# Kernel optimization log

Measured on AMD Instinct MI355X. Metric: run time of the kernel, lower is better.

Reference implementation:

```python
import jax, jax.numpy as jnp
import numpy as np

NA, NP_, E = 40000, 60000, 80000
D, H = 512, 8
DK = D // H
SQRT_DK = float(DK) ** 0.5


def setup_inputs() -> dict:
    key = jax.random.key(0)
    ks = list(jax.random.split(key, 20))
    it = iter(ks)

    def nrm(shape, scale=1.0):
        return jax.random.normal(next(it), shape, dtype=jnp.float32) * scale

    xav = (6.0 / (DK + DK)) ** 0.5  # xavier_uniform bound for (dk, dk)
    w_scale = D ** -0.5
    inp = {
        "h_author": nrm((NA, D)),
        "h_paper": nrm((NP_, D)),
        "writes_src": jax.random.randint(next(it), (E,), 0, NA, dtype=jnp.int32),
        "writes_dst": jax.random.randint(next(it), (E,), 0, NP_, dtype=jnp.int32),
        "cites_src": jax.random.randint(next(it), (E,), 0, NP_, dtype=jnp.int32),
        "cites_dst": jax.random.randint(next(it), (E,), 0, NP_, dtype=jnp.int32),
        "wb_src": jax.random.randint(next(it), (E,), 0, NP_, dtype=jnp.int32),
        "wb_dst": jax.random.randint(next(it), (E,), 0, NA, dtype=jnp.int32),
        # per-node-type linear weights (2 types: 0=author, 1=paper)
        "Wk": nrm((2, D, D), w_scale), "bk": jnp.zeros((2, D), jnp.float32),
        "Wq": nrm((2, D, D), w_scale), "bq": jnp.zeros((2, D), jnp.float32),
        "Wv": nrm((2, D, D), w_scale), "bv": jnp.zeros((2, D), jnp.float32),
        "Wa": nrm((2, D, D), w_scale), "ba": jnp.zeros((2, D), jnp.float32),
        # per-relation params (3 relations: 0=writes, 1=cites, 2=written_by)
        "rel_att": jax.random.uniform(next(it), (3, H, DK, DK), jnp.float32, -xav, xav),
        "rel_msg": jax.random.uniform(next(it), (3, H, DK, DK), jnp.float32, -xav, xav),
        "rel_pri": jnp.ones((3, H), jnp.float32),
        "skip": jnp.ones((2,), jnp.float32),
    }
    return inp


def _edge_attn_agg(k, q, v, src, dst, pri, n_dst):
    # k, v: (N_src, H, DK) relation-transformed; q: (N_dst, H, DK)
    s = jnp.einsum('ehd,ehd->eh', q[dst], k[src]) * pri / SQRT_DK  # (E, H)
    m = jax.ops.segment_max(s, dst, num_segments=n_dst)            # edge softmax by dst
    ex = jnp.exp(s - m[dst])
    den = jax.ops.segment_sum(ex, dst, num_segments=n_dst)
    a = ex / den[dst]
    return jax.ops.segment_sum(v[src] * a[:, :, None], dst, num_segments=n_dst)


def reference(h_author, h_paper, writes_src, writes_dst, cites_src, cites_dst,
              wb_src, wb_dst, Wk, bk, Wq, bq, Wv, bv, Wa, ba,
              rel_att, rel_msg, rel_pri, skip):
    def proj(h, W, b, t):
        return (h @ W[t] + b[t]).reshape(-1, H, DK)

    k_a, v_a, q_a = proj(h_author, Wk, bk, 0), proj(h_author, Wv, bv, 0), proj(h_author, Wq, bq, 0)
    k_p, v_p, q_p = proj(h_paper, Wk, bk, 1), proj(h_paper, Wv, bv, 1), proj(h_paper, Wq, bq, 1)

    def rel(k, v, r):
        return (jnp.einsum('nhd,hde->nhe', k, rel_att[r]),
                jnp.einsum('nhd,hde->nhe', v, rel_msg[r]))

    k0, v0 = rel(k_a, v_a, 0)  # writes: author -> paper
    agg_w = _edge_attn_agg(k0, q_p, v0, writes_src, writes_dst, rel_pri[0], NP_)
    k1, v1 = rel(k_p, v_p, 1)  # cites: paper -> paper
    agg_c = _edge_attn_agg(k1, q_p, v1, cites_src, cites_dst, rel_pri[1], NP_)
    k2, v2 = rel(k_p, v_p, 2)  # written_by: paper -> author
    agg_b = _edge_attn_agg(k2, q_a, v2, wb_src, wb_dst, rel_pri[2], NA)

    t_paper = ((agg_w + agg_c) * 0.5).reshape(NP_, D)  # cross_reducer='mean'
    t_author = agg_b.reshape(NA, D)

    alpha = jax.nn.sigmoid(skip)
    out_a = (t_author @ Wa[0] + ba[0]) * alpha[0] + h_author * (1.0 - alpha[0])
    out_p = (t_paper @ Wa[1] + ba[1]) * alpha[1] + h_paper * (1.0 - alpha[1])
    return out_a, out_p
```

## Files before the change

kernel.cpp:

```cpp
#include <hip/hip_runtime.h>
#include <math.h>

#define D_ 512
#define H_ 8

typedef short bf16x8 __attribute__((ext_vector_type(8)));
typedef float f32x4 __attribute__((ext_vector_type(4)));

struct Outs { void* p[5]; };

__device__ __forceinline__ unsigned short f2bf(float x) {
  unsigned int u = __float_as_uint(x);
  unsigned int r = (u + 0x7fff + ((u >> 16) & 1)) >> 16;
  return (unsigned short)r;
}
__device__ __forceinline__ float bf2f(unsigned short b) {
  return __uint_as_float(((unsigned int)b) << 16);
}

__global__ void fill_kernel(float* __restrict__ p, float v, long n) {
  long i = (long)blockIdx.x * blockDim.x + threadIdx.x;
  long st = (long)gridDim.x * blockDim.x;
  for (; i < n; i += st) p[i] = v;
}

__global__ void convert_bf16_kernel(const float* __restrict__ in,
                                    unsigned short* __restrict__ out, long n8) {
  long i = (long)blockIdx.x * blockDim.x + threadIdx.x;
  long st = (long)gridDim.x * blockDim.x;
  for (; i < n8; i += st) {
    float4 a = ((const float4*)in)[i * 2];
    float4 b = ((const float4*)in)[i * 2 + 1];
    bf16x8 o;
    o[0] = (short)f2bf(a.x); o[1] = (short)f2bf(a.y);
    o[2] = (short)f2bf(a.z); o[3] = (short)f2bf(a.w);
    o[4] = (short)f2bf(b.x); o[5] = (short)f2bf(b.y);
    o[6] = (short)f2bf(b.z); o[7] = (short)f2bf(b.w);
    ((bf16x8*)out)[i] = o;
  }
}

__global__ void transpose_bf16_kernel(const float* __restrict__ W,
                                      unsigned short* __restrict__ Wt) {
  int n = blockIdx.x;
  int k = threadIdx.x;
  Wt[(long)n * D_ + k] = f2bf(W[(long)k * D_ + n]);
}

__global__ void copy_bias_kernel(const float* __restrict__ in,
                                 float* __restrict__ out) {
  out[threadIdx.x] = in[threadIdx.x];
}

__global__ void fuse_weight_kernel(const float* __restrict__ Win,
                                   const float* __restrict__ bin,
                                   const float* __restrict__ rel,
                                   unsigned short* __restrict__ Wf,
                                   float* __restrict__ bf) {
  int row = blockIdx.x;
  int j = threadIdx.x;
  int h = j >> 6, e = j & 63;
  const float* src = (row < D_) ? (Win + (long)row * D_) : bin;
  const float* rl = rel + h * 64 * 64;
  float acc = 0.f;
#pragma unroll 16
  for (int d = 0; d < 64; ++d) acc = fmaf(src[h * 64 + d], rl[d * 64 + e], acc);
  if (row < D_) Wf[(long)j * D_ + row] = f2bf(acc);
  else bf[j] = acc;
}

__global__ void hist_kernel(const int* __restrict__ w_dst,
                            const int* __restrict__ c_dst,
                            const int* __restrict__ b_dst,
                            int* __restrict__ degree, int E, int NP) {
  int i = blockIdx.x * blockDim.x + threadIdx.x;
  if (i >= 3 * E) return;
  int r = i / E, e = i - r * E;
  int d, base;
  if (r == 0)      { d = w_dst[e]; base = 0; }
  else if (r == 1) { d = c_dst[e]; base = NP; }
  else             { d = b_dst[e]; base = 2 * NP; }
  atomicAdd(degree + base + d, 1);
}

__global__ void scan1_kernel(const int* __restrict__ in, int* __restrict__ out,
                             int* __restrict__ aux, int n) {
  __shared__ int tmp[256];
  int t = threadIdx.x;
  int i = blockIdx.x * 256 + t;
  int v = (i < n) ? in[i] : 0;
  tmp[t] = v;
  __syncthreads();
#pragma unroll
  for (int d = 1; d < 256; d <<= 1) {
    int add = (t >= d) ? tmp[t - d] : 0;
    __syncthreads();
    tmp[t] += add;
    __syncthreads();
  }
  if (i < n) out[i] = tmp[t] - v;
  if (t == 255) aux[blockIdx.x] = tmp[255];
}

__global__ void scan2_kernel(int* __restrict__ aux, int nb) {
  __shared__ int tmp[1024];
  int t = threadIdx.x;
  int v = (t < nb) ? aux[t] : 0;
  tmp[t] = v;
  __syncthreads();
#pragma unroll
  for (int d = 1; d < 1024; d <<= 1) {
    int add = (t >= d) ? tmp[t - d] : 0;
    __syncthreads();
    tmp[t] += add;
    __syncthreads();
  }
  if (t < nb) aux[t] = tmp[t] - v;
}

__global__ void scan3_kernel(int* __restrict__ starts, int* __restrict__ cursor,
                             const int* __restrict__ aux, int n) {
  int i = blockIdx.x * 256 + threadIdx.x;
  if (i >= n) return;
  int s = starts[i] + aux[blockIdx.x];
  starts[i] = s;
  cursor[i] = s;
}

__global__ void scatter_kernel(const int* __restrict__ w_src, const int* __restrict__ w_dst,
                               const int* __restrict__ c_src, const int* __restrict__ c_dst,
                               const int* __restrict__ b_src, const int* __restrict__ b_dst,
                               int* __restrict__ cursor, int* __restrict__ csr,
                               int E, int NP) {
  int i = blockIdx.x * blockDim.x + threadIdx.x;
  if (i >= 3 * E) return;
  int r = i / E, e = i - r * E;
  int s, d, base;
  if (r == 0)      { s = w_src[e]; d = w_dst[e]; base = 0; }
  else if (r == 1) { s = c_src[e]; d = c_dst[e]; base = NP; }
  else             { s = b_src[e]; d = b_dst[e]; base = 2 * NP; }
  int pos = atomicAdd(cursor + base + d, 1);
  csr[pos] = s;
}

template <int TWO_LISTS>
__global__ __launch_bounds__(256) void attn_kernel(
    const unsigned short* __restrict__ q,
    const unsigned short* __restrict__ k0, const unsigned short* __restrict__ v0,
    const unsigned short* __restrict__ k1, const unsigned short* __restrict__ v1,
    const int* __restrict__ csr, const int* __restrict__ starts,
    const int* __restrict__ degree, int base0, int base1,
    const float* __restrict__ pri, int poff0, int poff1,
    unsigned short* __restrict__ out, int n_nodes, float outscale) {
  int gw = (int)(((long)blockIdx.x * blockDim.x + threadIdx.x) >> 6);
  if (gw >= n_nodes) return;
  int lane = threadIdx.x & 63;
  int h = lane >> 3, off = (lane & 7) << 3;
  const long rowoff = (long)gw * D_ + h * 64 + off;
  bf16x8 qv = *(const bf16x8*)(q + rowoff);
  float qf[8];
#pragma unroll
  for (int r = 0; r < 8; ++r) qf[r] = bf2f((unsigned short)qv[r]);

  float res[8] = {};

  auto process = [&](const unsigned short* K, const unsigned short* V,
                     int base, float ps) {
    int st = starts[base + gw], dg = degree[base + gw];
    float m = -INFINITY, l = 0.f;
    float acc[8] = {};
    for (int i = 0; i < dg; ++i) {
      int s = csr[st + i];
      const long ro = (long)s * D_ + h * 64 + off;
      bf16x8 kv = *(const bf16x8*)(K + ro);
      bf16x8 vv = *(const bf16x8*)(V + ro);
      float dot = 0.f;
#pragma unroll
      for (int r = 0; r < 8; ++r)
        dot = fmaf(qf[r], bf2f((unsigned short)kv[r]), dot);
      dot += __shfl_xor(dot, 1);
      dot += __shfl_xor(dot, 2);
      dot += __shfl_xor(dot, 4);
      float sc = dot * ps;
      float mn = fmaxf(m, sc);
      float scale = __expf(m - mn);
      float p = __expf(sc - mn);
      l = l * scale + p;
#pragma unroll
      for (int r = 0; r < 8; ++r)
        acc[r] = acc[r] * scale + p * bf2f((unsigned short)vv[r]);
      m = mn;
    }
    if (l > 0.f) {
      float inv = 1.f / l;
#pragma unroll
      for (int r = 0; r < 8; ++r) res[r] += acc[r] * inv;
    }
  };

  process(k0, v0, base0, pri[poff0 + h] * 0.125f);
  if (TWO_LISTS) process(k1, v1, base1, pri[poff1 + h] * 0.125f);

  bf16x8 o;
#pragma unroll
  for (int r = 0; r < 8; ++r) o[r] = (short)f2bf(res[r] * outscale);
  *(bf16x8*)(out + rowoff) = o;
}

__device__ __forceinline__ void gload_lds16(const void* g, void* l) {
  __builtin_amdgcn_global_load_lds(
      (const __attribute__((address_space(1))) void*)g,
      (__attribute__((address_space(3))) void*)l, 16, 0, 0);
}

template <int OUT_BF16, int WITH_SKIP>
__global__ __launch_bounds__(512, 2) void gemm_mfma(
    const unsigned short* __restrict__ A,
    const unsigned short* __restrict__ Bt,
    const float* __restrict__ bias,
    Outs outs, int M, int GX, float a_scale,
    const float* __restrict__ Hres,
    const float* __restrict__ skip, int skip_idx) {
  __shared__ unsigned short Asm[2][256 * 64];
  __shared__ unsigned short Bsm[2][256 * 64];

  const int nwg = gridDim.x;
  const int orig = blockIdx.x;
  const int q8 = nwg >> 3, r8 = nwg & 7;
  const int xcd = orig & 7, pos = orig >> 3;
  const int wgid =
      (xcd < r8 ? xcd * (q8 + 1) : r8 * (q8 + 1) + (xcd - r8) * q8) + pos;
  const int bm = (wgid / GX) * 256;
  const int bn = (wgid % GX) * 256;

  const int tid = threadIdx.x;
  const int wave = tid >> 6, lane = tid & 63;
  const int wm = (wave >> 2) * 128;
  const int wn = (wave & 3) * 64;
  const int srow = tid >> 3;
  const int swz = ((tid & 7) ^ (srow & 7)) * 8;

  f32x4 acc[8][4] = {};

  const int rr = lane & 15;
  const int rx = (rr & 7) << 4;

  auto STAGE = [&](int buf, int kt) {
    const int k0 = kt * 64;
#pragma unroll
    for (int i = 0; i < 4; ++i) {
      int gr = bm + srow + i * 64;
      if (gr >= M) gr = M - 1;
      gload_lds16(A + (long)gr * D_ + k0 + swz, &Asm[buf][i * 4096 + wave * 512]);
    }
#pragma unroll
    for (int i = 0; i < 4; ++i) {
      int gr = bn + srow + i * 64;
      gload_lds16(Bt + (long)gr * D_ + k0 + swz, &Bsm[buf][i * 4096 + wave * 512]);
    }
  };

  STAGE(0, 0);
  STAGE(1, 1);

#pragma unroll
  for (int t = 0; t < 8; ++t) {
    const int p = t & 1;
    if (t == 7) asm volatile("s_waitcnt vmcnt(0)" ::: "memory");
    else        asm volatile("s_waitcnt vmcnt(8)" ::: "memory");
    __builtin_amdgcn_s_barrier();
    asm volatile("" ::: "memory");

#pragma unroll
    for (int kk = 0; kk < 2; ++kk) {
      const int cb = kk * 64 + (lane >> 4) * 16;
      const int cs = cb ^ rx;
      bf16x8 af[8], bfr[4];
#pragma unroll
      for (int mi = 0; mi < 8; ++mi)
        af[mi] = *(const bf16x8*)((const char*)&Asm[p][0] +
                                  (wm + mi * 16 + rr) * 128 + cs);
#pragma unroll
      for (int nj = 0; nj < 4; ++nj)
        bfr[nj] = *(const bf16x8*)((const char*)&Bsm[p][0] +
                                   (wn + nj * 16 + rr) * 128 + cs);
      __builtin_amdgcn_s_setprio(1);
#pragma unroll
      for (int mi = 0; mi < 8; ++mi)
#pragma unroll
        for (int nj = 0; nj < 4; ++nj)
          acc[mi][nj] = __builtin_amdgcn_mfma_f32_16x16x32_bf16(
              af[mi], bfr[nj], acc[mi][nj], 0, 0, 0);
      __builtin_amdgcn_s_setprio(0);
    }

    asm volatile("" ::: "memory");
    __builtin_amdgcn_s_barrier();
    asm volatile("" ::: "memory");
    if (t + 2 < 8) STAGE(p, t + 2);
  }

  float alpha = 1.f, beta = 0.f;
  if (WITH_SKIP) {
    float sv = skip[skip_idx];
    alpha = 1.f / (1.f + expf(-sv));
    beta = 1.f - alpha;
  }
  const int cr = (lane >> 4) * 4;
  const int cc = lane & 15;
  const int matu = (bn + wn) >> 9;
  const int wcb = (bn + wn) & 511;
  unsigned short* ob16 = (unsigned short*)outs.p[matu];
  float* ob32 = (float*)outs.p[0];
#pragma unroll
  for (int mi = 0; mi < 8; ++mi) {
    int rowb = bm + wm + mi * 16 + cr;
#pragma unroll
    for (int nj = 0; nj < 4; ++nj) {
      int col = bn + wn + nj * 16 + cc;
      float bb = bias[col];
#pragma unroll
      for (int r = 0; r < 4; ++r) {
        int row = rowb + r;
        if (row >= M) continue;
        float val = acc[mi][nj][r] * a_scale + bb;
        if (WITH_SKIP) val = val * alpha + Hres[(long)row * D_ + col] * beta;
        if (OUT_BF16)
          ob16[(long)row * D_ + wcb + nj * 16 + cc] = f2bf(val);
        else
          ob32[(long)row * D_ + col] = val;
      }
    }
  }
}

extern "C" void kernel_launch(void* const* d_in, const int* in_sizes, int n_in,
                              void* d_out, int out_size, void* d_ws, size_t ws_size,
                              hipStream_t stream) {
  const float* h_author = (const float*)d_in[0];
  const float* h_paper  = (const float*)d_in[1];
  const int* w_src = (const int*)d_in[2];
  const int* w_dst = (const int*)d_in[3];
  const int* c_src = (const int*)d_in[4];
  const int* c_dst = (const int*)d_in[5];
  const int* b_src = (const int*)d_in[6];
  const int* b_dst = (const int*)d_in[7];
  const float* Wk = (const float*)d_in[8];
  const float* bk = (const float*)d_in[9];
  const float* Wq = (const float*)d_in[10];
  const float* bq = (const float*)d_in[11];
  const float* Wv = (const float*)d_in[12];
  const float* bv = (const float*)d_in[13];
  const float* Wa = (const float*)d_in[14];
  const float* ba = (const float*)d_in[15];
  const float* rel_att = (const float*)d_in[16];
  const float* rel_msg = (const float*)d_in[17];
  const float* rel_pri = (const float*)d_in[18];
  const float* skip = (const float*)d_in[19];

  const int NA = in_sizes[0] / D_;
  const int NP = in_sizes[1] / D_;
  const int E  = in_sizes[2];
  const long nmax = (NA > NP) ? NA : NP;
  const int NT = 2 * NP + NA;

  char* w = (char*)d_ws;
  auto alloc = [&](long bytes) {
    char* p = w;
    w += (bytes + 255) & ~255L;
    return p;
  };
  unsigned short* hA16 = (unsigned short*)alloc((long)NA * D_ * 2);
  unsigned short* hP16 = (unsigned short*)alloc((long)NP * D_ * 2);
  unsigned short* Pq   = (unsigned short*)alloc((long)NP * D_ * 2);
  unsigned short* Pkc  = (unsigned short*)alloc((long)NP * D_ * 2);
  unsigned short* Pvc  = (unsigned short*)alloc((long)NP * D_ * 2);
  unsigned short* Pkb  = (unsigned short*)alloc((long)NP * D_ * 2);
  unsigned short* Pvb  = (unsigned short*)alloc((long)NP * D_ * 2);
  unsigned short* Aq   = (unsigned short*)alloc((long)NA * D_ * 2);
  unsigned short* Akw  = (unsigned short*)alloc((long)NA * D_ * 2);
  unsigned short* Avw  = (unsigned short*)alloc((long)NA * D_ * 2);
  unsigned short* t16  = (unsigned short*)alloc(nmax * D_ * 2);
  unsigned short* BtP  = (unsigned short*)alloc((long)2560 * D_ * 2);
  unsigned short* BtA  = (unsigned short*)alloc((long)1536 * D_ * 2);
  float* bfP           = (float*)alloc(2560 * 4);
  float* bfA           = (float*)alloc(1536 * 4);
  unsigned short* Wa0t = (unsigned short*)alloc((long)D_ * D_ * 2);
  unsigned short* Wa1t = (unsigned short*)alloc((long)D_ * D_ * 2);
  int* degree          = (int*)alloc((long)NT * 4);
  int* starts          = (int*)alloc((long)NT * 4);
  int* cursor          = (int*)alloc((long)NT * 4);
  int* csr             = (int*)alloc((long)3 * E * 4);
  int* aux             = (int*)alloc(((long)NT / 256 + 2) * 4);

  const long WD = (long)D_ * D_;
  const long RS = (long)H_ * 64 * 64;
  const long SEG = (long)D_ * D_;

  auto fill = [&](float* p, float v, long n) {
    long b = (n + 255) / 256;
    int blocks = (int)(b > 4096 ? 4096 : b);
    fill_kernel<<<blocks, 256, 0, stream>>>(p, v, n);
  };
  auto cvt = [&](const float* in, unsigned short* out, long n) {
    long n8 = n / 8;
    long b = (n8 + 255) / 256;
    int blocks = (int)(b > 2048 ? 2048 : b);
    convert_bf16_kernel<<<blocks, 256, 0, stream>>>(in, out, n8);
  };

  float* out_a = (float*)d_out;
  float* out_p = out_a + (long)NA * D_;

  cvt(h_author, hA16, (long)NA * D_);
  cvt(h_paper, hP16, (long)NP * D_);

  fill((float*)degree, 0.f, NT);
  {
    int th = 3 * E;
    hist_kernel<<<(th + 255) / 256, 256, 0, stream>>>(w_dst, c_dst, b_dst,
                                                      degree, E, NP);
    int nb = (NT + 255) / 256;
    scan1_kernel<<<nb, 256, 0, stream>>>(degree, starts, aux, NT);
    scan2_kernel<<<1, 1024, 0, stream>>>(aux, nb);
    scan3_kernel<<<nb, 256, 0, stream>>>(starts, cursor, aux, NT);
    scatter_kernel<<<(th + 255) / 256, 256, 0, stream>>>(
        w_src, w_dst, c_src, c_dst, b_src, b_dst, cursor, csr, E, NP);
  }

  transpose_bf16_kernel<<<D_, D_, 0, stream>>>(Wq + WD, BtP);
  copy_bias_kernel<<<1, D_, 0, stream>>>(bq + D_, bfP);
  fuse_weight_kernel<<<513, 512, 0, stream>>>(Wk + WD, bk + D_, rel_att + RS,
                                              BtP + SEG, bfP + 512);
  fuse_weight_kernel<<<513, 512, 0, stream>>>(Wv + WD, bv + D_, rel_msg + RS,
                                              BtP + 2 * SEG, bfP + 1024);
  fuse_weight_kernel<<<513, 512, 0, stream>>>(Wk + WD, bk + D_, rel_att + 2 * RS,
                                              BtP + 3 * SEG, bfP + 1536);
  fuse_weight_kernel<<<513, 512, 0, stream>>>(Wv + WD, bv + D_, rel_msg + 2 * RS,
                                              BtP + 4 * SEG, bfP + 2048);

  transpose_bf16_kernel<<<D_, D_, 0, stream>>>(Wq, BtA);
  copy_bias_kernel<<<1, D_, 0, stream>>>(bq, bfA);
  fuse_weight_kernel<<<513, 512, 0, stream>>>(Wk, bk, rel_att,
                                              BtA + SEG, bfA + 512);
  fuse_weight_kernel<<<513, 512, 0, stream>>>(Wv, bv, rel_msg,
                                              BtA + 2 * SEG, bfA + 1024);

  transpose_bf16_kernel<<<D_, D_, 0, stream>>>(Wa, Wa0t);
  transpose_bf16_kernel<<<D_, D_, 0, stream>>>(Wa + WD, Wa1t);

  {
    Outs o; o.p[0] = Pq; o.p[1] = Pkc; o.p[2] = Pvc; o.p[3] = Pkb; o.p[4] = Pvb;
    int gy = (NP + 255) / 256;
    gemm_mfma<1, 0><<<10 * gy, 512, 0, stream>>>(
        hP16, BtP, bfP, o, NP, 10, 1.f, nullptr, nullptr, 0);
  }
  {
    Outs o; o.p[0] = Aq; o.p[1] = Akw; o.p[2] = Avw; o.p[3] = Aq; o.p[4] = Aq;
    int gy = (NA + 255) / 256;
    gemm_mfma<1, 0><<<6 * gy, 512, 0, stream>>>(
        hA16, BtA, bfA, o, NA, 6, 1.f, nullptr, nullptr, 0);
  }

  {
    long th = (long)NP * 64;
    attn_kernel<1><<<(int)((th + 255) / 256), 256, 0, stream>>>(
        Pq, Akw, Avw, Pkc, Pvc, csr, starts, degree, 0, NP,
        rel_pri, 0, H_, t16, NP, 0.5f);
  }
  {
    Outs o; o.p[0] = out_p; o.p[1] = o.p[2] = o.p[3] = o.p[4] = out_p;
    int gy = (NP + 255) / 256;
    gemm_mfma<0, 1><<<2 * gy, 512, 0, stream>>>(
        t16, Wa1t, ba + D_, o, NP, 2, 1.f, h_paper, skip, 1);
  }

  {
    long th = (long)NA * 64;
    attn_kernel<0><<<(int)((th + 255) / 256), 256, 0, stream>>>(
        Aq, Pkb, Pvb, Pkb, Pvb, csr, starts, degree, 2 * NP, 2 * NP,
        rel_pri, 2 * H_, 2 * H_, t16, NA, 1.f);
  }
  {
    Outs o; o.p[0] = out_a; o.p[1] = o.p[2] = o.p[3] = o.p[4] = out_a;
    int gy = (NA + 255) / 256;
    gemm_mfma<0, 1><<<2 * gy, 512, 0, stream>>>(
        t16, Wa0t, ba, o, NA, 2, 1.f, h_author, skip, 0);
  }
}
```

Before: 985.5 us.

## Deepen MFMA GEMM LDS pipeline to 3-ahead half-K stages with one barrier

Splits each 64-wide K tile of the bf16 MFMA GEMM into two 32-wide halves held in four LDS slots. It prefetches three stages ahead and issues the next global-to-LDS load right after fragment reads, so only one barrier per step remains instead of two. The LDS layout changes to 64-byte rows with a new XOR swizzle. The aim is to hide global load latency better and cut synchronisation stalls. The costs are more loop iterations with smaller MFMA batches per barrier, plus possible bank-conflict changes from the new swizzle.

```diff
diff --git a/kernel.cpp b/kernel.cpp
--- a/kernel.cpp
+++ b/kernel.cpp
@@ -221,8 +221,8 @@
     Outs outs, int M, int GX, float a_scale,
     const float* __restrict__ Hres,
     const float* __restrict__ skip, int skip_idx) {
-  __shared__ unsigned short Asm[2][256 * 64];
-  __shared__ unsigned short Bsm[2][256 * 64];
+  __shared__ unsigned short AsmL[4 * 8192];
+  __shared__ unsigned short BsmL[4 * 8192];
 
   const int nwg = gridDim.x;
   const int orig = blockIdx.x;
@@ -237,67 +237,73 @@
   const int wave = tid >> 6, lane = tid & 63;
   const int wm = (wave >> 2) * 128;
   const int wn = (wave & 3) * 64;
-  const int srow = tid >> 3;
-  const int swz = ((tid & 7) ^ (srow & 7)) * 8;
+
+  const int srow = tid >> 2;
+  const int schk = tid & 3;
+  const int sf = ((tid >> 2) & 3) ^ ((tid >> 4) & 3);
+  const int scg = ((schk ^ sf) << 3);
+
+  const int rr = lane & 15;
+  const int qk = lane >> 4;
+  const int slotx = ((qk ^ (rr & 3) ^ ((rr >> 2) & 3)) << 4);
 
   f32x4 acc[8][4] = {};
 
-  const int rr = lane & 15;
-  const int rx = (rr & 7) << 4;
-
-  auto STAGE = [&](int buf, int kt) {
-    const int k0 = kt * 64;
-#pragma unroll
-    for (int i = 0; i < 4; ++i) {
-      int gr = bm + srow + i * 64;
+  auto STAGE_U = [&](int u) {
+    const int tile = u >> 1, kh = u & 1;
+    const int slot = ((tile & 1) * 2 + kh);
+    const int k0 = tile * 64 + kh * 32 + scg;
+#pragma unroll
+    for (int rd = 0; rd < 2; ++rd) {
+      int gr = bm + srow + rd * 128;
       if (gr >= M) gr = M - 1;
-      gload_lds16(A + (long)gr * D_ + k0 + swz, &Asm[buf][i * 4096 + wave * 512]);
+      gload_lds16(A + (long)gr * D_ + k0,
+                  AsmL + slot * 8192 + rd * 4096 + wave * 512);
     }
 #pragma unroll
-    for (int i = 0; i < 4; ++i) {
-      int gr = bn + srow + i * 64;
-      gload_lds16(Bt + (long)gr * D_ + k0 + swz, &Bsm[buf][i * 4096 + wave * 512]);
+    for (int rd = 0; rd < 2; ++rd) {
+      int gr = bn + srow + rd * 128;
+      gload_lds16(Bt + (long)gr * D_ + k0,
+                  BsmL + slot * 8192 + rd * 4096 + wave * 512);
     }
   };
 
-  STAGE(0, 0);
-  STAGE(1, 1);
-
-#pragma unroll
-  for (int t = 0; t < 8; ++t) {
-    const int p = t & 1;
-    if (t == 7) asm volatile("s_waitcnt vmcnt(0)" ::: "memory");
-    else        asm volatile("s_waitcnt vmcnt(8)" ::: "memory");
+  STAGE_U(0);
+  STAGE_U(1);
+  STAGE_U(2);
+
+#pragma unroll
+  for (int s = 0; s < 16; ++s) {
+    if (s <= 13)      asm volatile("s_waitcnt vmcnt(8)" ::: "memory");
+    else if (s == 14) asm volatile("s_waitcnt vmcnt(4)" ::: "memory");
+    else              asm volatile("s_waitcnt vmcnt(0)" ::: "memory");
     __builtin_amdgcn_s_barrier();
     asm volatile("" ::: "memory");
 
-#pragma unroll
-    for (int kk = 0; kk < 2; ++kk) {
-      const int cb = kk * 64 + (lane >> 4) * 16;
-      const int cs = cb ^ rx;
-      bf16x8 af[8], bfr[4];
-#pragma unroll
-      for (int mi = 0; mi < 8; ++mi)
-        af[mi] = *(const bf16x8*)((const char*)&Asm[p][0] +
-                                  (wm + mi * 16 + rr) * 128 + cs);
+    const int tile = s >> 1, kh = s & 1;
+    const int slot = ((tile & 1) * 2 + kh);
+    const char* ab = (const char*)AsmL + slot * 16384;
+    const char* bb = (const char*)BsmL + slot * 16384;
+
+    bf16x8 af[8], bfr[4];
+#pragma unroll
+    for (int mi = 0; mi < 8; ++mi)
+      af[mi] = *(const bf16x8*)(ab + (wm + mi * 16 + rr) * 64 + slotx);
+#pragma unroll
+    for (int nj = 0; nj < 4; ++nj)
+      bfr[nj] = *(const bf16x8*)(bb + (wn + nj * 16 + rr) * 64 + slotx);
+
+    if (s + 3 <= 15) STAGE_U(s + 3);
+
+    __builtin_amdgcn_s_setprio(1);
+#pragma unroll
+    for (int mi = 0; mi < 8; ++mi)
 #pragma unroll
       for (int nj = 0; nj < 4; ++nj)
-        bfr[nj] = *(const bf16x8*)((const char*)&Bsm[p][0] +
-                                   (wn + nj * 16 + rr) * 128 + cs);
-      __builtin_amdgcn_s_setprio(1);
-#pragma unroll
-      for (int mi = 0; mi < 8; ++mi)
-#pragma unroll
-        for (int nj = 0; nj < 4; ++nj)
-          acc[mi][nj] = __builtin_amdgcn_mfma_f32_16x16x32_bf16(
-              af[mi], bfr[nj], acc[mi][nj], 0, 0, 0);
-      __builtin_amdgcn_s_setprio(0);
-    }
-
+        acc[mi][nj] = __builtin_amdgcn_mfma_f32_16x16x32_bf16(
+            af[mi], bfr[nj], acc[mi][nj], 0, 0, 0);
+    __builtin_amdgcn_s_setprio(0);
     asm volatile("" ::: "memory");
-    __builtin_amdgcn_s_barrier();
-    asm volatile("" ::: "memory");
-    if (t + 2 < 8) STAGE(p, t + 2);
   }
 
   float alpha = 1.f, beta = 0.f;
@@ -318,12 +324,12 @@
 #pragma unroll
     for (int nj = 0; nj < 4; ++nj) {
       int col = bn + wn + nj * 16 + cc;
-      float bb = bias[col];
+      float bb2 = bias[col];
 #pragma unroll
       for (int r = 0; r < 4; ++r) {
         int row = rowb + r;
         if (row >= M) continue;
-        float val = acc[mi][nj][r] * a_scale + bb;
+        float val = acc[mi][nj][r] * a_scale + bb2;
         if (WITH_SKIP) val = val * alpha + Hres[(long)row * D_ + col] * beta;
         if (OUT_BF16)
           ob16[(long)row * D_ + wcb + nj * 16 + cc] = f2bf(val);
```

After: 1.002 ms. About the same (+1.6%).

## Merge prep, projection, attention and output launches into grouped kernels

Applied to the files above, without the earlier changes.

Folds the bf16 conversions, weight fusion, transposes, bias copies and degree zeroing into one multi-role prep kernel. The two projection GEMMs, the two attention passes and the two output GEMMs each become a single grouped launch. A padded shared t16 buffer lets author and paper rows coexist. This cuts launch count and tail under-utilisation, at the cost of more complex index dispatch and a larger workspace.

```diff
diff --git a/kernel.cpp b/kernel.cpp
--- a/kernel.cpp
+++ b/kernel.cpp
@@ -6,8 +6,6 @@
 
 typedef short bf16x8 __attribute__((ext_vector_type(8)));
 typedef float f32x4 __attribute__((ext_vector_type(4)));
-
-struct Outs { void* p[5]; };
 
 __device__ __forceinline__ unsigned short f2bf(float x) {
   unsigned int u = __float_as_uint(x);
@@ -18,55 +16,58 @@
   return __uint_as_float(((unsigned int)b) << 16);
 }
 
-__global__ void fill_kernel(float* __restrict__ p, float v, long n) {
-  long i = (long)blockIdx.x * blockDim.x + threadIdx.x;
-  long st = (long)gridDim.x * blockDim.x;
-  for (; i < n; i += st) p[i] = v;
-}
-
-__global__ void convert_bf16_kernel(const float* __restrict__ in,
-                                    unsigned short* __restrict__ out, long n8) {
-  long i = (long)blockIdx.x * blockDim.x + threadIdx.x;
-  long st = (long)gridDim.x * blockDim.x;
-  for (; i < n8; i += st) {
+struct PrepArgs {
+  const float *hA, *hP;
+  unsigned short *hA16, *hP16;
+  const float *fWin[6], *fbin[6], *frel[6];
+  unsigned short *fWf[6];
+  float *fbf[6];
+  const float *tW[4];
+  unsigned short *tWt[4];
+  const float *cin[2];
+  float *cout[2];
+  int *degree;
+  int NT;
+  int b1, b2, b3, b4, b5;
+};
+
+__global__ __launch_bounds__(512) void prep_kernel(PrepArgs p) {
+  const int b = blockIdx.x, t = threadIdx.x;
+  if (b < p.b2) {
+    const float* in; unsigned short* out; long i;
+    if (b < p.b1) { in = p.hA; out = p.hA16; i = (long)b * 512 + t; }
+    else          { in = p.hP; out = p.hP16; i = (long)(b - p.b1) * 512 + t; }
     float4 a = ((const float4*)in)[i * 2];
-    float4 b = ((const float4*)in)[i * 2 + 1];
+    float4 c = ((const float4*)in)[i * 2 + 1];
     bf16x8 o;
     o[0] = (short)f2bf(a.x); o[1] = (short)f2bf(a.y);
     o[2] = (short)f2bf(a.z); o[3] = (short)f2bf(a.w);
-    o[4] = (short)f2bf(b.x); o[5] = (short)f2bf(b.y);
-    o[6] = (short)f2bf(b.z); o[7] = (short)f2bf(b.w);
+    o[4] = (short)f2bf(c.x); o[5] = (short)f2bf(c.y);
+    o[6] = (short)f2bf(c.z); o[7] = (short)f2bf(c.w);
     ((bf16x8*)out)[i] = o;
-  }
-}
-
-__global__ void transpose_bf16_kernel(const float* __restrict__ W,
-                                      unsigned short* __restrict__ Wt) {
-  int n = blockIdx.x;
-  int k = threadIdx.x;
-  Wt[(long)n * D_ + k] = f2bf(W[(long)k * D_ + n]);
-}
-
-__global__ void copy_bias_kernel(const float* __restrict__ in,
-                                 float* __restrict__ out) {
-  out[threadIdx.x] = in[threadIdx.x];
-}
-
-__global__ void fuse_weight_kernel(const float* __restrict__ Win,
-                                   const float* __restrict__ bin,
-                                   const float* __restrict__ rel,
-                                   unsigned short* __restrict__ Wf,
-                                   float* __restrict__ bf) {
-  int row = blockIdx.x;
-  int j = threadIdx.x;
-  int h = j >> 6, e = j & 63;
-  const float* src = (row < D_) ? (Win + (long)row * D_) : bin;
-  const float* rl = rel + h * 64 * 64;
-  float acc = 0.f;
+  } else if (b < p.b3) {
+    int idx = b - p.b2;
+    int job = idx / 513, row = idx - job * 513;
+    int h = t >> 6, e = t & 63;
+    const float* src = (row < D_) ? (p.fWin[job] + (long)row * D_) : p.fbin[job];
+    const float* rl = p.frel[job] + h * 64 * 64;
+    float acc = 0.f;
 #pragma unroll 16
-  for (int d = 0; d < 64; ++d) acc = fmaf(src[h * 64 + d], rl[d * 64 + e], acc);
-  if (row < D_) Wf[(long)j * D_ + row] = f2bf(acc);
-  else bf[j] = acc;
+    for (int d = 0; d < 64; ++d)
+      acc = fmaf(src[h * 64 + d], rl[d * 64 + e], acc);
+    if (row < D_) p.fWf[job][(long)t * D_ + row] = f2bf(acc);
+    else p.fbf[job][t] = acc;
+  } else if (b < p.b4) {
+    int idx = b - p.b3;
+    int job = idx >> 9, n = idx & 511;
+    p.tWt[job][(long)n * D_ + t] = f2bf(p.tW[job][(long)t * D_ + n]);
+  } else if (b < p.b5) {
+    int job = b - p.b4;
+    p.cout[job][t] = p.cin[job][t];
+  } else {
+    int i = (b - p.b5) * 512 + t;
+    if (i < p.NT) p.degree[i] = 0;
+  }
 }
 
 __global__ void hist_kernel(const int* __restrict__ w_dst,
@@ -143,21 +144,42 @@
   csr[pos] = s;
 }
 
-template <int TWO_LISTS>
-__global__ __launch_bounds__(256) void attn_kernel(
-    const unsigned short* __restrict__ q,
-    const unsigned short* __restrict__ k0, const unsigned short* __restrict__ v0,
-    const unsigned short* __restrict__ k1, const unsigned short* __restrict__ v1,
+__global__ __launch_bounds__(256) void attn_all(
+    const unsigned short* __restrict__ Pq,
+    const unsigned short* __restrict__ Akw, const unsigned short* __restrict__ Avw,
+    const unsigned short* __restrict__ Pkc, const unsigned short* __restrict__ Pvc,
+    const unsigned short* __restrict__ Aq,
+    const unsigned short* __restrict__ Pkb, const unsigned short* __restrict__ Pvb,
     const int* __restrict__ csr, const int* __restrict__ starts,
-    const int* __restrict__ degree, int base0, int base1,
-    const float* __restrict__ pri, int poff0, int poff1,
-    unsigned short* __restrict__ out, int n_nodes, float outscale) {
-  int gw = (int)(((long)blockIdx.x * blockDim.x + threadIdx.x) >> 6);
-  if (gw >= n_nodes) return;
+    const int* __restrict__ degree, const float* __restrict__ pri,
+    unsigned short* __restrict__ t16, int NP, int NA, int NAp) {
+  long gid = (long)blockIdx.x * blockDim.x + threadIdx.x;
+  int gw = (int)(gid >> 6);
+  if (gw >= NP + NAp) return;
   int lane = threadIdx.x & 63;
   int h = lane >> 3, off = (lane & 7) << 3;
-  const long rowoff = (long)gw * D_ + h * 64 + off;
-  bf16x8 qv = *(const bf16x8*)(q + rowoff);
+
+  const unsigned short* q;
+  long orow;
+  int node;
+  const int paper = gw < NP;
+  if (paper) {
+    node = gw; q = Pq;
+    orow = (long)(NAp + node) * D_ + h * 64 + off;
+  } else {
+    int aw = gw - NP;
+    orow = (long)aw * D_ + h * 64 + off;
+    if (aw >= NA) {
+      bf16x8 z;
+#pragma unroll
+      for (int r = 0; r < 8; ++r) z[r] = 0;
+      *(bf16x8*)(t16 + orow) = z;
+      return;
+    }
+    node = aw; q = Aq;
+  }
+
+  bf16x8 qv = *(const bf16x8*)(q + (long)node * D_ + h * 64 + off);
   float qf[8];
 #pragma unroll
   for (int r = 0; r < 8; ++r) qf[r] = bf2f((unsigned short)qv[r]);
@@ -165,8 +187,8 @@
   float res[8] = {};
 
   auto process = [&](const unsigned short* K, const unsigned short* V,
-                     int base, float ps) {
-    int st = starts[base + gw], dg = degree[base + gw];
+                     int nodeabs, float ps) {
+    int st = starts[nodeabs], dg = degree[nodeabs];
     float m = -INFINITY, l = 0.f;
     float acc[8] = {};
     for (int i = 0; i < dg; ++i) {
@@ -184,11 +206,11 @@
       float sc = dot * ps;
       float mn = fmaxf(m, sc);
       float scale = __expf(m - mn);
-      float p = __expf(sc - mn);
-      l = l * scale + p;
+      float pv = __expf(sc - mn);
+      l = l * scale + pv;
 #pragma unroll
       for (int r = 0; r < 8; ++r)
-        acc[r] = acc[r] * scale + p * bf2f((unsigned short)vv[r]);
+        acc[r] = acc[r] * scale + pv * bf2f((unsigned short)vv[r]);
       m = mn;
     }
     if (l > 0.f) {
@@ -198,13 +220,20 @@
     }
   };
 
-  process(k0, v0, base0, pri[poff0 + h] * 0.125f);
-  if (TWO_LISTS) process(k1, v1, base1, pri[poff1 + h] * 0.125f);
+  float outscale;
+  if (paper) {
+    process(Akw, Avw, node, pri[h] * 0.125f);
+    process(Pkc, Pvc, NP + node, pri[8 + h] * 0.125f);
+    outscale = 0.5f;
+  } else {
+    process(Pkb, Pvb, 2 * NP + node, pri[16 + h] * 0.125f);
+    outscale = 1.0f;
+  }
 
   bf16x8 o;
 #pragma unroll
   for (int r = 0; r < 8; ++r) o[r] = (short)f2bf(res[r] * outscale);
-  *(bf16x8*)(out + rowoff) = o;
+  *(bf16x8*)(t16 + orow) = o;
 }
 
 __device__ __forceinline__ void gload_lds16(const void* g, void* l) {
@@ -213,25 +242,32 @@
       (__attribute__((address_space(3))) void*)l, 16, 0, 0);
 }
 
-template <int OUT_BF16, int WITH_SKIP>
-__global__ __launch_bounds__(512, 2) void gemm_mfma(
-    const unsigned short* __restrict__ A,
-    const unsigned short* __restrict__ Bt,
-    const float* __restrict__ bias,
-    Outs outs, int M, int GX, float a_scale,
-    const float* __restrict__ Hres,
-    const float* __restrict__ skip, int skip_idx) {
+struct ProjArgs {
+  const unsigned short *A0, *A1;
+  const unsigned short *B0, *B1;
+  const float *bias0, *bias1;
+  void* outs[8];
+  int M0, M1, split;
+};
+
+__global__ __launch_bounds__(512, 2) void gemm_proj(ProjArgs pa) {
   __shared__ unsigned short Asm[2][256 * 64];
   __shared__ unsigned short Bsm[2][256 * 64];
 
-  const int nwg = gridDim.x;
-  const int orig = blockIdx.x;
+  const int nwg = gridDim.x, orig = blockIdx.x;
   const int q8 = nwg >> 3, r8 = nwg & 7;
   const int xcd = orig & 7, pos = orig >> 3;
   const int wgid =
       (xcd < r8 ? xcd * (q8 + 1) : r8 * (q8 + 1) + (xcd - r8) * q8) + pos;
-  const int bm = (wgid / GX) * 256;
-  const int bn = (wgid % GX) * 256;
+
+  int reg, mt, nt;
+  if (wgid < pa.split) { reg = 0; mt = wgid / 6; nt = wgid - mt * 6; }
+  else { int r = wgid - pa.split; reg = 1; mt = r / 10; nt = r - mt * 10; }
+  const unsigned short* A  = reg ? pa.A1 : pa.A0;
+  const unsigned short* Bt = reg ? pa.B1 : pa.B0;
+  const float* bias = reg ? pa.bias1 : pa.bias0;
+  const int M = reg ? pa.M1 : pa.M0;
+  const int bm = mt * 256, bn = nt * 256;
 
   const int tid = threadIdx.x;
   const int wave = tid >> 6, lane = tid & 63;
@@ -241,7 +277,6 @@
   const int swz = ((tid & 7) ^ (srow & 7)) * 8;
 
   f32x4 acc[8][4] = {};
-
   const int rr = lane & 15;
   const int rx = (rr & 7) << 4;
 
@@ -262,7 +297,6 @@
 
   STAGE(0, 0);
   STAGE(1, 1);
-
 #pragma unroll
   for (int t = 0; t < 8; ++t) {
     const int p = t & 1;
@@ -300,18 +334,11 @@
     if (t + 2 < 8) STAGE(p, t + 2);
   }
 
-  float alpha = 1.f, beta = 0.f;
-  if (WITH_SKIP) {
-    float sv = skip[skip_idx];
-    alpha = 1.f / (1.f + expf(-sv));
-    beta = 1.f - alpha;
-  }
   const int cr = (lane >> 4) * 4;
   const int cc = lane & 15;
   const int matu = (bn + wn) >> 9;
   const int wcb = (bn + wn) & 511;
-  unsigned short* ob16 = (unsigned short*)outs.p[matu];
-  float* ob32 = (float*)outs.p[0];
+  unsigned short* ob16 = (unsigned short*)pa.outs[(reg ? 3 : 0) + matu];
 #pragma unroll
   for (int mi = 0; mi < 8; ++mi) {
     int rowb = bm + wm + mi * 16 + cr;
@@ -323,12 +350,130 @@
       for (int r = 0; r < 4; ++r) {
         int row = rowb + r;
         if (row >= M) continue;
-        float val = acc[mi][nj][r] * a_scale + bb;
-        if (WITH_SKIP) val = val * alpha + Hres[(long)row * D_ + col] * beta;
-        if (OUT_BF16)
-          ob16[(long)row * D_ + wcb + nj * 16 + cc] = f2bf(val);
-        else
-          ob32[(long)row * D_ + col] = val;
+        float val = acc[mi][nj][r] + bb;
+        ob16[(long)row * D_ + wcb + nj * 16 + cc] = f2bf(val);
+      }
+    }
+  }
+}
+
+struct OutArgs {
+  const unsigned short* A;
+  const unsigned short *B0, *B1;
+  const float *bias0, *bias1;
+  const float *H0, *H1;
+  const float* skip;
+  float *o0, *o1;
+  int mtsplit, NAp, M0, M1;
+};
+
+__global__ __launch_bounds__(512, 2) void gemm_out(OutArgs oa) {
+  __shared__ unsigned short Asm[2][256 * 64];
+  __shared__ unsigned short Bsm[2][256 * 64];
+
+  const int nwg = gridDim.x, orig = blockIdx.x;
+  const int q8 = nwg >> 3, r8 = nwg & 7;
+  const int xcd = orig & 7, pos = orig >> 3;
+  const int wgid =
+      (xcd < r8 ? xcd * (q8 + 1) : r8 * (q8 + 1) + (xcd - r8) * q8) + pos;
+
+  const int bmt = wgid >> 1;
+  const int bn = (wgid & 1) * 256;
+  const int reg = bmt >= oa.mtsplit;
+  const int bm = (reg ? bmt - oa.mtsplit : bmt) * 256;
+  const int abase = reg ? oa.NAp : 0;
+  const int M = reg ? oa.M1 : oa.M0;
+  const unsigned short* Bt = reg ? oa.B1 : oa.B0;
+  const float* bias = reg ? oa.bias1 : oa.bias0;
+  const float* Hres = reg ? oa.H1 : oa.H0;
+  float* outp = reg ? oa.o1 : oa.o0;
+
+  const int tid = threadIdx.x;
+  const int wave = tid >> 6, lane = tid & 63;
+  const int wm = (wave >> 2) * 128;
+  const int wn = (wave & 3) * 64;
+  const int srow = tid >> 3;
+  const int swz = ((tid & 7) ^ (srow & 7)) * 8;
+
+  f32x4 acc[8][4] = {};
+  const int rr = lane & 15;
+  const int rx = (rr & 7) << 4;
+
+  auto STAGE = [&](int buf, int kt) {
+    const int k0 = kt * 64;
+#pragma unroll
+    for (int i = 0; i < 4; ++i) {
+      int gr = bm + srow + i * 64;
+      if (gr >= M) gr = M - 1;
+      gload_lds16(oa.A + (long)(abase + gr) * D_ + k0 + swz,
+                  &Asm[buf][i * 4096 + wave * 512]);
+    }
+#pragma unroll
+    for (int i = 0; i < 4; ++i) {
+      int gr = bn + srow + i * 64;
+      gload_lds16(Bt + (long)gr * D_ + k0 + swz,
+                  &Bsm[buf][i * 4096 + wave * 512]);
+    }
+  };
+
+  STAGE(0, 0);
+  STAGE(1, 1);
+#pragma unroll
+  for (int t = 0; t < 8; ++t) {
+    const int p = t & 1;
+    if (t == 7) asm volatile("s_waitcnt vmcnt(0)" ::: "memory");
+    else        asm volatile("s_waitcnt vmcnt(8)" ::: "memory");
+    __builtin_amdgcn_s_barrier();
+    asm volatile("" ::: "memory");
+
+#pragma unroll
+    for (int kk = 0; kk < 2; ++kk) {
+      const int cb = kk * 64 + (lane >> 4) * 16;
+      const int cs = cb ^ rx;
+      bf16x8 af[8], bfr[4];
+#pragma unroll
+      for (int mi = 0; mi < 8; ++mi)
+        af[mi] = *(const bf16x8*)((const char*)&Asm[p][0] +
+                                  (wm + mi * 16 + rr) * 128 + cs);
+#pragma unroll
+      for (int nj = 0; nj < 4; ++nj)
+        bfr[nj] = *(const bf16x8*)((const char*)&Bsm[p][0] +
+                                   (wn + nj * 16 + rr) * 128 + cs);
+      __builtin_amdgcn_s_setprio(1);
+#pragma unroll
+      for (int mi = 0; mi < 8; ++mi)
+#pragma unroll
+        for (int nj = 0; nj < 4; ++nj)
+          acc[mi][nj] = __builtin_amdgcn_mfma_f32_16x16x32_bf16(
+              af[mi], bfr[nj], acc[mi][nj], 0, 0, 0);
+      __builtin_amdgcn_s_setprio(0);
+    }
+
+    asm volatile("" ::: "memory");
+    __builtin_amdgcn_s_barrier();
+    asm volatile("" ::: "memory");
+    if (t + 2 < 8) STAGE(p, t + 2);
+  }
+
+  float sv = oa.skip[reg];
+  float alpha = 1.f / (1.f + expf(-sv));
+  float beta = 1.f - alpha;
+  const int cr = (lane >> 4) * 4;
+  const int cc = lane & 15;
+#pragma unroll
+  for (int mi = 0; mi < 8; ++mi) {
+    int rowb = bm + wm + mi * 16 + cr;
+#pragma unroll
+    for (int nj = 0; nj < 4; ++nj) {
+      int col = bn + wn + nj * 16 + cc;
+      float bb = bias[col];
+#pragma unroll
+      for (int r = 0; r < 4; ++r) {
+        int row = rowb + r;
+        if (row >= M) continue;
+        float val = acc[mi][nj][r] + bb;
+        val = val * alpha + Hres[(long)row * D_ + col] * beta;
+        outp[(long)row * D_ + col] = val;
       }
     }
   }
@@ -361,8 +506,10 @@
   const int NA = in_sizes[0] / D_;
   const int NP = in_sizes[1] / D_;
   const int E  = in_sizes[2];
-  const long nmax = (NA > NP) ? NA : NP;
   const int NT = 2 * NP + NA;
+  const int tA = (NA + 255) / 256;
+  const int tP = (NP + 255) / 256;
+  const int NAp = tA * 256;
 
   char* w = (char*)d_ws;
   auto alloc = [&](long bytes) {
@@ -380,7 +527,7 @@
   unsigned short* Aq   = (unsigned short*)alloc((long)NA * D_ * 2);
   unsigned short* Akw  = (unsigned short*)alloc((long)NA * D_ * 2);
   unsigned short* Avw  = (unsigned short*)alloc((long)NA * D_ * 2);
-  unsigned short* t16  = (unsigned short*)alloc(nmax * D_ * 2);
+  unsigned short* t16  = (unsigned short*)alloc((long)(NAp + NP) * D_ * 2);
   unsigned short* BtP  = (unsigned short*)alloc((long)2560 * D_ * 2);
   unsigned short* BtA  = (unsigned short*)alloc((long)1536 * D_ * 2);
   float* bfP           = (float*)alloc(2560 * 4);
@@ -397,25 +544,40 @@
   const long RS = (long)H_ * 64 * 64;
   const long SEG = (long)D_ * D_;
 
-  auto fill = [&](float* p, float v, long n) {
-    long b = (n + 255) / 256;
-    int blocks = (int)(b > 4096 ? 4096 : b);
-    fill_kernel<<<blocks, 256, 0, stream>>>(p, v, n);
-  };
-  auto cvt = [&](const float* in, unsigned short* out, long n) {
-    long n8 = n / 8;
-    long b = (n8 + 255) / 256;
-    int blocks = (int)(b > 2048 ? 2048 : b);
-    convert_bf16_kernel<<<blocks, 256, 0, stream>>>(in, out, n8);
-  };
-
   float* out_a = (float*)d_out;
   float* out_p = out_a + (long)NA * D_;
 
-  cvt(h_author, hA16, (long)NA * D_);
-  cvt(h_paper, hP16, (long)NP * D_);
-
-  fill((float*)degree, 0.f, NT);
+  {
+    PrepArgs p;
+    p.hA = h_author; p.hP = h_paper; p.hA16 = hA16; p.hP16 = hP16;
+    p.fWin[0] = Wk + WD; p.fbin[0] = bk + D_; p.frel[0] = rel_att + RS;
+    p.fWf[0] = BtP + SEG;     p.fbf[0] = bfP + 512;
+    p.fWin[1] = Wv + WD; p.fbin[1] = bv + D_; p.frel[1] = rel_msg + RS;
+    p.fWf[1] = BtP + 2 * SEG; p.fbf[1] = bfP + 1024;
+    p.fWin[2] = Wk + WD; p.fbin[2] = bk + D_; p.frel[2] = rel_att + 2 * RS;
+    p.fWf[2] = BtP + 3 * SEG; p.fbf[2] = bfP + 1536;
+    p.fWin[3] = Wv + WD; p.fbin[3] = bv + D_; p.frel[3] = rel_msg + 2 * RS;
+    p.fWf[3] = BtP + 4 * SEG; p.fbf[3] = bfP + 2048;
+    p.fWin[4] = Wk;      p.fbin[4] = bk;      p.frel[4] = rel_att;
+    p.fWf[4] = BtA + SEG;     p.fbf[4] = bfA + 512;
+    p.fWin[5] = Wv;      p.fbin[5] = bv;      p.frel[5] = rel_msg;
+    p.fWf[5] = BtA + 2 * SEG; p.fbf[5] = bfA + 1024;
+    p.tW[0] = Wq + WD; p.tWt[0] = BtP;
+    p.tW[1] = Wq;      p.tWt[1] = BtA;
+    p.tW[2] = Wa;      p.tWt[2] = Wa0t;
+    p.tW[3] = Wa + WD; p.tWt[3] = Wa1t;
+    p.cin[0] = bq + D_; p.cout[0] = bfP;
+    p.cin[1] = bq;      p.cout[1] = bfA;
+    p.degree = degree; p.NT = NT;
+    p.b1 = NA / 8;
+    p.b2 = p.b1 + NP / 8;
+    p.b3 = p.b2 + 6 * 513;
+    p.b4 = p.b3 + 4 * 512;
+    p.b5 = p.b4 + 2;
+    int total = p.b5 + (NT + 511) / 512;
+    prep_kernel<<<total, 512, 0, stream>>>(p);
+  }
+
   {
     int th = 3 * E;
     hist_kernel<<<(th + 255) / 256, 256, 0, stream>>>(w_dst, c_dst, b_dst,
@@ -428,63 +590,37 @@
         w_src, w_dst, c_src, c_dst, b_src, b_dst, cursor, csr, E, NP);
   }
 
-  transpose_bf16_kernel<<<D_, D_, 0, stream>>>(Wq + WD, BtP);
-  copy_bias_kernel<<<1, D_, 0, stream>>>(bq + D_, bfP);
-  fuse_weight_kernel<<<513, 512, 0, stream>>>(Wk + WD, bk + D_, rel_att + RS,
-                                              BtP + SEG, bfP + 512);
-  fuse_weight_kernel<<<513, 512, 0, stream>>>(Wv + WD, bv + D_, rel_msg + RS,
-                                              BtP + 2 * SEG, bfP + 1024);
-  fuse_weight_kernel<<<513, 512, 0, stream>>>(Wk + WD, bk + D_, rel_att + 2 * RS,
-                                              BtP + 3 * SEG, bfP + 1536);
-  fuse_weight_kernel<<<513, 512, 0, stream>>>(Wv + WD, bv + D_, rel_msg + 2 * RS,
-                                              BtP + 4 * SEG, bfP + 2048);
-
-  transpose_bf16_kernel<<<D_, D_, 0, stream>>>(Wq, BtA);
-  copy_bias_kernel<<<1, D_, 0, stream>>>(bq, bfA);
-  fuse_weight_kernel<<<513, 512, 0, stream>>>(Wk, bk, rel_att,
-                                              BtA + SEG, bfA + 512);
-  fuse_weight_kernel<<<513, 512, 0, stream>>>(Wv, bv, rel_msg,
-                                              BtA + 2 * SEG, bfA + 1024);
-
-  transpose_bf16_kernel<<<D_, D_, 0, stream>>>(Wa, Wa0t);
-  transpose_bf16_kernel<<<D_, D_, 0, stream>>>(Wa + WD, Wa1t);
-
   {
-    Outs o; o.p[0] = Pq; o.p[1] = Pkc; o.p[2] = Pvc; o.p[3] = Pkb; o.p[4] = Pvb;
-    int gy = (NP + 255) / 256;
-    gemm_mfma<1, 0><<<10 * gy, 512, 0, stream>>>(
-        hP16, BtP, bfP, o, NP, 10, 1.f, nullptr, nullptr, 0);
-  }
+    ProjArgs pa;
+    pa.A0 = hA16; pa.A1 = hP16;
+    pa.B0 = BtA;  pa.B1 = BtP;
+    pa.bias0 = bfA; pa.bias1 = bfP;
+    pa.outs[0] = Aq;  pa.outs[1] = Akw; pa.outs[2] = Avw;
+    pa.outs[3] = Pq;  pa.outs[4] = Pkc; pa.outs[5] = Pvc;
+    pa.outs[6] = Pkb; pa.outs[7] = Pvb;
+    pa.M0 = NA; pa.M1 = NP;
+    pa.split = tA * 6;
+    int nwg = pa.split + tP * 10;
+    gemm_proj<<<nwg, 512, 0, stream>>>(pa);
+  }
+
   {
-    Outs o; o.p[0] = Aq; o.p[1] = Akw; o.p[2] = Avw; o.p[3] = Aq; o.p[4] = Aq;
-    int gy = (NA + 255) / 256;
-    gemm_mfma<1, 0><<<6 * gy, 512, 0, stream>>>(
-        hA16, BtA, bfA, o, NA, 6, 1.f, nullptr, nullptr, 0);
+    long th = (long)(NP + NAp) * 64;
+    attn_all<<<(int)((th + 255) / 256), 256, 0, stream>>>(
+        Pq, Akw, Avw, Pkc, Pvc, Aq, Pkb, Pvb,
+        csr, starts, degree, rel_pri, t16, NP, NA, NAp);
   }
 
   {
-    long th = (long)NP * 64;
-    attn_kernel<1><<<(int)((th + 255) / 256), 256, 0, stream>>>(
-        Pq, Akw, Avw, Pkc, Pvc, csr, starts, degree, 0, NP,
-        rel_pri, 0, H_, t16, NP, 0.5f);
-  }
-  {
-    Outs o; o.p[0] = out_p; o.p[1] = o.p[2] = o.p[3] = o.p[4] = out_p;
-    int gy = (NP + 255) / 256;
-    gemm_mfma<0, 1><<<2 * gy, 512, 0, stream>>>(
-        t16, Wa1t, ba + D_, o, NP, 2, 1.f, h_paper, skip, 1);
-  }
-
-  {
-    long th = (long)NA * 64;
-    attn_kernel<0><<<(int)((th + 255) / 256), 256, 0, stream>>>(
-        Aq, Pkb, Pvb, Pkb, Pvb, csr, starts, degree, 2 * NP, 2 * NP,
-        rel_pri, 2 * H_, 2 * H_, t16, NA, 1.f);
-  }
-  {
-    Outs o; o.p[0] = out_a; o.p[1] = o.p[2] = o.p[3] = o.p[4] = out_a;
-    int gy = (NA + 255) / 256;
-    gemm_mfma<0, 1><<<2 * gy, 512, 0, stream>>>(
-        t16, Wa0t, ba, o, NA, 2, 1.f, h_author, skip, 0);
-  }
-}
+    OutArgs oa;
+    oa.A = t16;
+    oa.B0 = Wa0t; oa.B1 = Wa1t;
+    oa.bias0 = ba; oa.bias1 = ba + D_;
+    oa.H0 = h_author; oa.H1 = h_paper;
+    oa.skip = skip;
+    oa.o0 = out_a; oa.o1 = out_p;
+    oa.mtsplit = tA; oa.NAp = NAp; oa.M0 = NA; oa.M1 = NP;
+    int nwg = (tA + tP) * 2;
+    gemm_out<<<nwg, 512, 0, stream>>>(oa);
+  }
+}
```

New measurement: 919.0 us. -6.8%, faster.
